# Kernel tuning notes

Measured on AMD Instinct MI355X. Metric: run time of the kernel, lower is better.

Reference implementation:

```python
import jax, jax.numpy as jnp
import numpy as np

B, N, H, L, K, R = 1024, 64, 128, 4, 16, 20
CUTOFF = 5.0
GAMMA = 10.0   # RBF width
N_TYPES = 10

def _rn(k, shape, scale):
    return jax.random.normal(k, shape, jnp.float32) * scale

def setup_inputs():
    key = jax.random.key(0)
    ks = jax.random.split(key, 16)
    z = lambda *s: jnp.zeros(s, jnp.float32)
    return {
        "positions": _rn(ks[0], (B, N, 3), 2.0),
        "atomic_numbers": jax.random.randint(ks[1], (B, N), 0, N_TYPES),
        "atom_embed": _rn(ks[2], (N_TYPES, H // 4), 0.1),
        "pos_W": _rn(ks[3], (3, 3 * H // 4), 0.5),
        "pos_b": z(3 * H // 4),
        "msg_W": _rn(ks[4], (L, 2 * H + R, H), (2 * H + R) ** -0.5),
        "msg_b": z(L, H),
        "upd_W": _rn(ks[5], (L, H, H), H ** -0.5),
        "upd_b": z(L, H),
        "gself_W": _rn(ks[6], (L, H, H), H ** -0.5),
        "gmean_W": _rn(ks[7], (L, H, H), H ** -0.5),
        "g_b": z(L, H),
        "fus_W": _rn(ks[8], (L, 2 * H, H), (2 * H) ** -0.5),
        "fus_b": z(L, H),
        "ln_g": jnp.ones((L, H), jnp.float32),
        "ln_b": z(L, H),
        "cb_W1": _rn(ks[9], (L, H, 4 * H), H ** -0.5),
        "cb_b1": z(L, 4 * H),
        "cb_W2": _rn(ks[10], (L, 4 * H, H), (4 * H) ** -0.5),
        "cb_b2": z(L, H),
        "fo_W1": _rn(ks[11], (H, H), H ** -0.5),
        "fo_b1": z(H),
        "fo_W2": _rn(ks[12], (H, 3), H ** -0.5),
        "fo_b2": z(3),
    }

def _ln(x, g, b):
    m = x.mean(-1, keepdims=True)
    v = ((x - m) ** 2).mean(-1, keepdims=True)
    return (x - m) * jax.lax.rsqrt(v + 1e-5) * g + b

def reference(positions, atomic_numbers, atom_embed, pos_W, pos_b, msg_W, msg_b,
              upd_W, upd_b, gself_W, gmean_W, g_b, fus_W, fus_b, ln_g, ln_b,
              cb_W1, cb_b1, cb_W2, cb_b2, fo_W1, fo_b1, fo_W2, fo_b2):
    silu = jax.nn.silu
    Bb, Nn, _ = positions.shape
    # embeddings: atom type (H/4) || position (3H/4)
    h = jnp.concatenate([atom_embed[atomic_numbers], positions @ pos_W + pos_b], -1)  # [B,N,H]
    # kNN graph from positions (static across layers since positions are fixed)
    diff = positions[:, :, None, :] - positions[:, None, :, :]
    d2 = jnp.sum(diff * diff, -1) + jnp.eye(Nn, dtype=positions.dtype) * 1e9  # exclude self
    neg_d2, idx = jax.lax.top_k(-d2, K)                       # [B,N,K]
    d = jnp.sqrt(jnp.maximum(-neg_d2, 1e-12))
    centers = jnp.linspace(0.0, CUTOFF, R).astype(positions.dtype)
    rbf = jnp.exp(-GAMMA * (d[..., None] - centers) ** 2)     # [B,N,K,R]
    env = (0.5 * (jnp.cos(jnp.pi * d / CUTOFF) + 1.0) * (d < CUTOFF))[..., None]  # cosine cutoff
    idx_flat = idx.reshape(Bb, Nn * K)
    for i in range(msg_W.shape[0]):
        # local MPNN: gather neighbors, message MLP on [h_i, h_j, rbf], envelope, sum
        h_j = jnp.take_along_axis(h, idx_flat[:, :, None], axis=1).reshape(Bb, Nn, K, -1)
        h_i = jnp.broadcast_to(h[:, :, None, :], h_j.shape)
        m = silu(jnp.concatenate([h_i, h_j, rbf], -1) @ msg_W[i] + msg_b[i]) * env
        local = h + silu(m.sum(2) @ upd_W[i] + upd_b[i])
        # Clifford mean-field: self transform + global-mean transform
        glob = silu(h @ gself_W[i] + h.mean(1, keepdims=True) @ gmean_W[i] + g_b[i])
        # fusion (dropout is identity at inference)
        fused = silu(jnp.concatenate([local, glob], -1) @ fus_W[i] + fus_b[i])
        # Clifford block: pre-LN residual MLP
        x = _ln(fused, ln_g[i], ln_b[i])
        h = fused + silu(x @ cb_W1[i] + cb_b1[i]) @ cb_W2[i] + cb_b2[i]
    return silu(h @ fo_W1 + fo_b1) @ fo_W2 + fo_b2  # [B,N,3] forces
```

## Files before the change

### kernel.cpp

```cpp
#include <hip/hip_runtime.h>

typedef unsigned short ushort_t;
typedef unsigned int uint_t;
typedef unsigned long long ull_t;
typedef __attribute__((ext_vector_type(8))) short short8;
typedef __attribute__((ext_vector_type(4))) float f32x4;

#define B_ 1024
#define N_ 64
#define H_ 128
#define NT 512

#define IMG_WI 0
#define IMG_WJ 16384
#define IMG_UW 32768
#define IMG_GS 49152
#define IMG_FT 65536
#define IMG_FB 81920
#define IMG_C1 98304
#define IMG_C2 163840
#define IMG_GMT 229376
#define IMG_RW 245760
#define IMG_L 249856
#define IMG_FO 999424
#define WS_WEIGHTS (2u*1024u*1024u)
#define KNN_STRIDE 12288u

__device__ __forceinline__ ushort_t f2bf(float f) {
    uint_t u = __float_as_uint(f);
    return (ushort_t)((u + 0x7fffu + ((u >> 16) & 1u)) >> 16);
}
__device__ __forceinline__ float bf2f(ushort_t u) {
    union { uint_t i; float f; } v; v.i = ((uint_t)u) << 16; return v.f;
}
__device__ __forceinline__ float siluf(float x) { return x / (1.0f + __expf(-x)); }

__device__ __forceinline__ int sidx(int m, int k) {
    return m * H_ + (((k >> 3) ^ (m & 7)) << 3) + (k & 7);
}
__device__ __forceinline__ int fragoff(int m, int ch) {
    return m * H_ + ((ch ^ (m & 7)) << 3);
}

extern "C" __global__ __launch_bounds__(256)
void convert_weights(const float* __restrict__ msg_W, const float* __restrict__ upd_W,
                     const float* __restrict__ gself_W, const float* __restrict__ fus_W,
                     const float* __restrict__ cb_W1, const float* __restrict__ cb_W2,
                     const float* __restrict__ gmean_W, const float* __restrict__ fo_W1,
                     ushort_t* __restrict__ wimg)
{
    const int g = blockIdx.x;
    if (g >= 244) {
        int st = g - 244;
        ushort_t* dst = wimg + IMG_FO + st * 4096;
        for (int e = 0; e < 16; ++e) {
            int q = threadIdx.x * 16 + e;
            int n = q >> 7, k = q & 127;
            dst[q] = f2bf(fo_W1[(size_t)k * 128 + st * 32 + n]);
        }
        return;
    }
    const int l = g / 61, r = g - l * 61;
    ushort_t* base = wimg + l * IMG_L;
    if (r == 60) {
        const float* W = msg_W + l * 35328 + 256 * 128;
        ushort_t* dst = base + IMG_RW;
        for (int e = 0; e < 16; ++e) {
            int q = threadIdx.x * 16 + e;
            int sub = q >> 10, n = (q >> 5) & 31, k = q & 31;
            dst[q] = f2bf(k < 20 ? W[(size_t)k * 128 + sub * 32 + n] : 0.0f);
        }
        return;
    }
    const float* W; int ld = 128, k0 = 0, c0, off, st;
    if      (r < 4)  { W = msg_W + l * 35328;            st = r;      off = IMG_WI;  c0 = st * 32; }
    else if (r < 8)  { W = msg_W + l * 35328;  k0 = 128; st = r - 4;  off = IMG_WJ;  c0 = st * 32; }
    else if (r < 12) { W = upd_W + l * 16384;            st = r - 8;  off = IMG_UW;  c0 = st * 32; }
    else if (r < 16) { W = gself_W + l * 16384;          st = r - 12; off = IMG_GS;  c0 = st * 32; }
    else if (r < 20) { W = fus_W + l * 32768;            st = r - 16; off = IMG_FT;  c0 = st * 32; }
    else if (r < 24) { W = fus_W + l * 32768;  k0 = 128; st = r - 20; off = IMG_FB;  c0 = st * 32; }
    else if (r < 40) { W = cb_W1 + l * 65536;  ld = 512; st = r - 24; off = IMG_C1;  c0 = st * 32; }
    else if (r < 56) { int j = (r - 40) >> 2; W = cb_W2 + l * 65536; k0 = j * 128;
                       st = r - 40; off = IMG_C2; c0 = ((r - 40) & 3) * 32; }
    else             { W = gmean_W + l * 16384;          st = r - 56; off = IMG_GMT; c0 = st * 32; }
    ushort_t* dst = base + off + st * 4096;
    for (int e = 0; e < 16; ++e) {
        int q = threadIdx.x * 16 + e;
        int n = q >> 7, k = q & 127;
        dst[q] = f2bf(W[(size_t)(k0 + k) * ld + c0 + n]);
    }
}

extern "C" __global__ __launch_bounds__(64)
void knn_kernel(const float* __restrict__ positions, char* __restrict__ ws)
{
    const int b = blockIdx.x, lane = threadIdx.x;
    float px = positions[b * 192 + lane * 3 + 0];
    float py = positions[b * 192 + lane * 3 + 1];
    float pz = positions[b * 192 + lane * 3 + 2];
    float* kd = (float*)(ws + WS_WEIGHTS + (size_t)b * KNN_STRIDE);
    float* ke = kd + 1024;
    ushort_t* ki = (ushort_t*)(ke + 1024);
    for (int n = 0; n < 64; ++n) {
        float dx = __fsub_rn(__shfl(px, n), px);
        float dy = __fsub_rn(__shfl(py, n), py);
        float dz = __fsub_rn(__shfl(pz, n), pz);
        float d2 = __fadd_rn(__fadd_rn(__fmul_rn(dx, dx), __fmul_rn(dy, dy)), __fmul_rn(dz, dz));
        if (lane == n) d2 = 1e30f;
        float sd = 0.f; int si = 0;
        for (int k = 0; k < 16; ++k) {
            float dmin = d2;
            #pragma unroll
            for (int o = 1; o < 64; o <<= 1) dmin = fminf(dmin, __shfl_xor(dmin, o));
            ull_t mask = __ballot(d2 == dmin);
            int widx = __ffsll(mask) - 1;
            if (lane == widx) d2 = 1e30f;
            if (lane == k) { si = widx; sd = dmin; }
        }
        if (lane < 16) {
            float dd = sqrtf(fmaxf(sd, 1e-12f));
            kd[n * 16 + lane] = dd;
            ke[n * 16 + lane] = (dd < 5.0f) ? 0.5f * (__cosf(0.62831853071795864769f * dd) + 1.0f) : 0.0f;
            ki[n * 16 + lane] = (ushort_t)si;
        }
    }
}

#define HFS 132
struct __align__(16) Smem {
    ushort_t T1[N_ * H_];
    ushort_t T2[N_ * H_];
    float Hf[N_ * HFS];
    float d[1024];
    float env[1024];
    ushort_t idx[1024];
    char u[2048];
};

__device__ __forceinline__ f32x4 gemm_s(const short8 a[4], const ushort_t* __restrict__ img,
                                        int s, int nl, int quad)
{
    short8 b0 = *(const short8*)(img + s * 4096 + nl * 128 + (0 * 4 + quad) * 8);
    short8 b1 = *(const short8*)(img + s * 4096 + nl * 128 + (1 * 4 + quad) * 8);
    short8 b2 = *(const short8*)(img + s * 4096 + nl * 128 + (2 * 4 + quad) * 8);
    short8 b3 = *(const short8*)(img + s * 4096 + nl * 128 + (3 * 4 + quad) * 8);
    f32x4 c = {0.f, 0.f, 0.f, 0.f};
    c = __builtin_amdgcn_mfma_f32_16x16x32_bf16(a[0], b0, c, 0, 0, 0);
    c = __builtin_amdgcn_mfma_f32_16x16x32_bf16(a[1], b1, c, 0, 0, 0);
    c = __builtin_amdgcn_mfma_f32_16x16x32_bf16(a[2], b2, c, 0, 0, 0);
    c = __builtin_amdgcn_mfma_f32_16x16x32_bf16(a[3], b3, c, 0, 0, 0);
    return c;
}
__device__ __forceinline__ f32x4 gemm_s_acc(const short8 a[4], const ushort_t* __restrict__ img,
                                            int s, int nl, int quad, f32x4 c)
{
    short8 b0 = *(const short8*)(img + s * 4096 + nl * 128 + (0 * 4 + quad) * 8);
    short8 b1 = *(const short8*)(img + s * 4096 + nl * 128 + (1 * 4 + quad) * 8);
    short8 b2 = *(const short8*)(img + s * 4096 + nl * 128 + (2 * 4 + quad) * 8);
    short8 b3 = *(const short8*)(img + s * 4096 + nl * 128 + (3 * 4 + quad) * 8);
    c = __builtin_amdgcn_mfma_f32_16x16x32_bf16(a[0], b0, c, 0, 0, 0);
    c = __builtin_amdgcn_mfma_f32_16x16x32_bf16(a[1], b1, c, 0, 0, 0);
    c = __builtin_amdgcn_mfma_f32_16x16x32_bf16(a[2], b2, c, 0, 0, 0);
    c = __builtin_amdgcn_mfma_f32_16x16x32_bf16(a[3], b3, c, 0, 0, 0);
    return c;
}
__device__ __forceinline__ void loadA(const ushort_t* __restrict__ X, int mrow, int quad, short8 a[4]) {
    #pragma unroll
    for (int kc = 0; kc < 4; ++kc) a[kc] = *(const short8*)&X[fragoff(mrow, kc * 4 + quad)];
}
__device__ __forceinline__ void buildA(const float* __restrict__ Hf, int mrow, int quad, short8 a[4]) {
    #pragma unroll
    for (int kc = 0; kc < 4; ++kc) {
        const float* p = Hf + mrow * HFS + (kc * 4 + quad) * 8;
        float4 u0 = *(const float4*)p;
        float4 u1 = *(const float4*)(p + 4);
        short8 v;
        v[0] = (short)f2bf(u0.x); v[1] = (short)f2bf(u0.y);
        v[2] = (short)f2bf(u0.z); v[3] = (short)f2bf(u0.w);
        v[4] = (short)f2bf(u1.x); v[5] = (short)f2bf(u1.y);
        v[6] = (short)f2bf(u1.z); v[7] = (short)f2bf(u1.w);
        a[kc] = v;
    }
}

extern "C" __global__ __launch_bounds__(NT, 4)
void md17_fused_kernel(
    const float* __restrict__ positions, const int* __restrict__ atomic_numbers,
    const float* __restrict__ atom_embed, const float* __restrict__ pos_W,
    const float* __restrict__ pos_b,
    const float* __restrict__ msg_b, const float* __restrict__ upd_b,
    const float* __restrict__ g_b, const float* __restrict__ fus_b,
    const float* __restrict__ ln_g, const float* __restrict__ ln_b,
    const float* __restrict__ cb_b1, const float* __restrict__ cb_b2,
    const float* __restrict__ fo_b1,
    const float* __restrict__ fo_W2, const float* __restrict__ fo_b2,
    char* __restrict__ ws, float* __restrict__ out)
{
    __shared__ Smem sm;
    const int b = blockIdx.x;
    const int tid = threadIdx.x;
    const int wave = tid >> 6, lane = tid & 63;
    const int quad = lane >> 4, l15 = lane & 15;
    const int Mt = wave >> 1;
    const int mrow = Mt * 16 + l15;
    const int nl = (wave & 1) * 16 + l15;

    const ushort_t* wimg = (const ushort_t*)ws;
    float* spos = (float*)sm.u;
    ushort_t* part = (ushort_t*)sm.u;
    float* hmean = (float*)(sm.u + 1024);
    float* gvec  = (float*)(sm.u + 1536);
    float2* lnb  = (float2*)sm.u;

    {
        const char* kb = ws + WS_WEIGHTS + (size_t)b * KNN_STRIDE;
        const float* kd = (const float*)kb;
        const float* ke = (const float*)(kb + 4096);
        const uint_t* ki = (const uint_t*)(kb + 8192);
        for (int t = tid; t < 1024; t += NT) { sm.d[t] = kd[t]; sm.env[t] = ke[t]; }
        ((uint_t*)sm.idx)[tid] = ki[tid];
        if (tid < 192) spos[tid] = positions[b * 192 + tid];
    }
    __syncthreads();

    for (int t = tid; t < N_ * H_; t += NT) {
        int n = t >> 7, f = t & 127;
        float v;
        if (f < 32) {
            v = atom_embed[atomic_numbers[b * N_ + n] * 32 + f];
        } else {
            int j = f - 32;
            v = pos_b[j];
            #pragma unroll
            for (int c = 0; c < 3; ++c)
                v = fmaf(spos[n * 3 + c], pos_W[c * 96 + j], v);
        }
        sm.Hf[n * HFS + f] = v;
        sm.T1[sidx(n, f)] = f2bf(v);
    }
    __syncthreads();

    #pragma unroll 1
    for (int l = 0; l < 4; ++l) {
        const ushort_t* wl = wimg + l * IMG_L;
        const float* mb  = msg_b + l * H_;
        const float* ub  = upd_b + l * H_;
        const float* gb  = g_b + l * H_;
        const float* fb  = fus_b + l * H_;
        const float* lg  = ln_g + l * H_;
        const float* lb  = ln_b + l * H_;
        const float* c1b = cb_b1 + l * 4 * H_;
        const float* c2b = cb_b2 + l * H_;

        short8 a_h[4];
        #pragma unroll
        for (int s = 0; s < 4; ++s) {
            int col = s * 32 + nl;
            const float* hp = sm.Hf + (Mt * 16 + quad * 4) * HFS + col;
            float p = hp[0] + hp[HFS] + hp[2 * HFS] + hp[3 * HFS];
            p += __shfl_xor(p, 16);
            p += __shfl_xor(p, 32);
            if (quad == 0) part[Mt * 128 + col] = f2bf(p);
        }
        loadA(sm.T1, mrow, quad, a_h);
        __syncthreads();

        if (tid < H_)
            hmean[tid] = (bf2f(part[tid]) + bf2f(part[128 + tid])
                        + bf2f(part[256 + tid]) + bf2f(part[384 + tid])) * (1.0f / 64.0f);
        __syncthreads();

        if (tid < H_) {
            float s = gb[tid];
            const ushort_t* wrow = wl + IMG_GMT + tid * 128;
            for (int c = 0; c < 128; c += 8) {
                short8 w = *(const short8*)(wrow + c);
                #pragma unroll
                for (int i = 0; i < 8; ++i) s = fmaf(hmean[c + i], bf2f((ushort_t)w[i]), s);
            }
            gvec[tid] = s;
        }
        #pragma unroll
        for (int s = 0; s < 4; ++s) {
            f32x4 c = gemm_s(a_h, wl + IMG_WI, s, nl, quad);
            int col = s * 32 + nl; float bv = mb[col];
            #pragma unroll
            for (int r = 0; r < 4; ++r)
                sm.T1[sidx(Mt * 16 + quad * 4 + r, col)] = f2bf(c[r] + bv);
        }
        #pragma unroll
        for (int s = 0; s < 4; ++s) {
            f32x4 c = gemm_s(a_h, wl + IMG_WJ, s, nl, quad);
            int col = s * 32 + nl;
            #pragma unroll
            for (int r = 0; r < 4; ++r)
                sm.T2[sidx(Mt * 16 + quad * 4 + r, col)] = f2bf(c[r]);
        }
        __syncthreads();

        {
            float ccv[8];
            #pragma unroll
            for (int j = 0; j < 8; ++j)
                ccv[j] = (float)((double)(quad * 8 + j) * (5.0 / 19.0));
            #pragma unroll 1
            for (int g = 0; g < 16; ++g) {
                int n = g * 4 + Mt;
                int jv[4]; float ev[4];
                #pragma unroll
                for (int r = 0; r < 4; ++r) {
                    int k = quad * 4 + r;
                    jv[r] = sm.idx[n * 16 + k];
                    ev[r] = sm.env[n * 16 + k];
                }
                float ddm = sm.d[n * 16 + l15];
                short8 arb;
                #pragma unroll
                for (int j = 0; j < 8; ++j) {
                    float t2 = ddm - ccv[j];
                    float rv = __expf(-10.0f * t2 * t2);
                    arb[j] = (short)((quad * 8 + j) < 20 ? f2bf(rv) : (ushort_t)0);
                }
                #pragma unroll
                for (int s = 0; s < 4; ++s) {
                    short8 brw = *(const short8*)(wl + IMG_RW + s * 1024 + nl * 32 + quad * 8);
                    f32x4 c = {0.f, 0.f, 0.f, 0.f};
                    c = __builtin_amdgcn_mfma_f32_16x16x32_bf16(arb, brw, c, 0, 0, 0);
                    int col = s * 32 + nl;
                    float ai = bf2f(sm.T1[sidx(n, col)]);
                    float acc = 0.f;
                    #pragma unroll
                    for (int r = 0; r < 4; ++r) {
                        float gm = bf2f(sm.T2[sidx(jv[r], col)]);
                        acc = fmaf(siluf(ai + gm + c[r]), ev[r], acc);
                    }
                    acc += __shfl_xor(acc, 16);
                    acc += __shfl_xor(acc, 32);
                    if (quad == 0) sm.T1[sidx(n, col)] = f2bf(acc);
                }
            }
        }
        __syncthreads();

        short8 a_m[4]; loadA(sm.T1, mrow, quad, a_m);
        __syncthreads();

        #pragma unroll
        for (int s = 0; s < 4; ++s) {
            f32x4 c = gemm_s(a_m, wl + IMG_UW, s, nl, quad);
            int col = s * 32 + nl; float bv = ub[col];
            #pragma unroll
            for (int r = 0; r < 4; ++r) {
                int row = Mt * 16 + quad * 4 + r;
                sm.T2[sidx(row, col)] = f2bf(sm.Hf[row * HFS + col] + siluf(c[r] + bv));
            }
        }
        {
            short8 a_hh[4]; buildA(sm.Hf, mrow, quad, a_hh);
            #pragma unroll
            for (int s = 0; s < 4; ++s) {
                f32x4 c = gemm_s(a_hh, wl + IMG_GS, s, nl, quad);
                int col = s * 32 + nl; float gv = gvec[col];
                #pragma unroll
                for (int r = 0; r < 4; ++r)
                    sm.T1[sidx(Mt * 16 + quad * 4 + r, col)] = f2bf(siluf(c[r] + gv));
            }
        }
        __syncthreads();

        {
            short8 a_t[4];
            loadA(sm.T2, mrow, quad, a_t);
            #pragma unroll
            for (int s = 0; s < 4; ++s) {
                f32x4 c = gemm_s(a_t, wl + IMG_FT, s, nl, quad);
                int col = s * 32 + nl;
                int rb = (Mt * 16 + quad * 4) * HFS + col;
                sm.Hf[rb] = c[0]; sm.Hf[rb + HFS] = c[1];
                sm.Hf[rb + 2 * HFS] = c[2]; sm.Hf[rb + 3 * HFS] = c[3];
            }
            loadA(sm.T1, mrow, quad, a_t);
            float sr0 = 0.f, sr1 = 0.f, sr2 = 0.f, sr3 = 0.f;
            float qr0 = 0.f, qr1 = 0.f, qr2 = 0.f, qr3 = 0.f;
            #pragma unroll
            for (int s = 0; s < 4; ++s) {
                f32x4 c = gemm_s(a_t, wl + IMG_FB, s, nl, quad);
                int col = s * 32 + nl; float bv = fb[col];
                int rb = (Mt * 16 + quad * 4) * HFS + col;
                float v0 = siluf(sm.Hf[rb] + c[0] + bv);
                float v1 = siluf(sm.Hf[rb + HFS] + c[1] + bv);
                float v2 = siluf(sm.Hf[rb + 2 * HFS] + c[2] + bv);
                float v3 = siluf(sm.Hf[rb + 3 * HFS] + c[3] + bv);
                sm.Hf[rb] = v0; sm.Hf[rb + HFS] = v1;
                sm.Hf[rb + 2 * HFS] = v2; sm.Hf[rb + 3 * HFS] = v3;
                sr0 += v0; sr1 += v1; sr2 += v2; sr3 += v3;
                qr0 += v0 * v0; qr1 += v1 * v1; qr2 += v2 * v2; qr3 += v3 * v3;
            }
            #pragma unroll
            for (int o = 1; o < 16; o <<= 1) {
                sr0 += __shfl_xor(sr0, o); qr0 += __shfl_xor(qr0, o);
                sr1 += __shfl_xor(sr1, o); qr1 += __shfl_xor(qr1, o);
                sr2 += __shfl_xor(sr2, o); qr2 += __shfl_xor(qr2, o);
                sr3 += __shfl_xor(sr3, o); qr3 += __shfl_xor(qr3, o);
            }
            if (l15 == 0) {
                int base = (Mt * 16 + quad * 4) * 2 + (wave & 1);
                lnb[base]     = make_float2(sr0, qr0);
                lnb[base + 2] = make_float2(sr1, qr1);
                lnb[base + 4] = make_float2(sr2, qr2);
                lnb[base + 6] = make_float2(sr3, qr3);
            }
        }
        __syncthreads();

        #pragma unroll
        for (int r = 0; r < 4; ++r) {
            int row = Mt * 16 + quad * 4 + r;
            float2 h0 = lnb[row * 2], h1 = lnb[row * 2 + 1];
            float mu = (h0.x + h1.x) * (1.0f / 128.0f);
            float var = (h0.y + h1.y) * (1.0f / 128.0f) - mu * mu;
            float rs = rsqrtf(var + 1e-5f);
            #pragma unroll
            for (int s = 0; s < 4; ++s) {
                int col = s * 32 + nl;
                sm.T1[sidx(row, col)] = f2bf((sm.Hf[row * HFS + col] - mu) * rs * lg[col] + lb[col]);
            }
        }
        __syncthreads();

        {
            f32x4 acc2[4];
            #pragma unroll
            for (int s = 0; s < 4; ++s) acc2[s] = (f32x4){0.f, 0.f, 0.f, 0.f};
            #pragma unroll 1
            for (int j = 0; j < 4; ++j) {
                {
                    short8 a_x[4]; loadA(sm.T1, mrow, quad, a_x);
                    #pragma unroll
                    for (int s = 0; s < 4; ++s) {
                        f32x4 c = gemm_s(a_x, wl + IMG_C1 + j * 16384, s, nl, quad);
                        int col = s * 32 + nl; float bv = c1b[j * H_ + col];
                        #pragma unroll
                        for (int r = 0; r < 4; ++r)
                            sm.T2[sidx(Mt * 16 + quad * 4 + r, col)] = f2bf(siluf(c[r] + bv));
                    }
                }
                __syncthreads();
                {
                    short8 a_t[4]; loadA(sm.T2, mrow, quad, a_t);
                    #pragma unroll
                    for (int s = 0; s < 4; ++s)
                        acc2[s] = gemm_s_acc(a_t, wl + IMG_C2 + j * 16384, s, nl, quad, acc2[s]);
                }
                __syncthreads();
            }

            #pragma unroll
            for (int s = 0; s < 4; ++s) {
                int col = s * 32 + nl; float bv = c2b[col];
                #pragma unroll
                for (int r = 0; r < 4; ++r) {
                    int row = Mt * 16 + quad * 4 + r;
                    float v = sm.Hf[row * HFS + col] + acc2[s][r] + bv;
                    sm.Hf[row * HFS + col] = v;
                    sm.T1[sidx(row, col)] = f2bf(v);
                }
            }
        }
        __syncthreads();
    }

    {
        short8 a_f[4]; loadA(sm.T1, mrow, quad, a_f);
        #pragma unroll
        for (int s = 0; s < 4; ++s) {
            f32x4 c = gemm_s(a_f, wimg + IMG_FO, s, nl, quad);
            int col = s * 32 + nl; float bv = fo_b1[col];
            #pragma unroll
            for (int r = 0; r < 4; ++r)
                sm.T2[sidx(Mt * 16 + quad * 4 + r, col)] = f2bf(siluf(c[r] + bv));
        }
    }
    __syncthreads();
    if (tid < N_ * 3) {
        int n = tid / 3, j = tid - n * 3;
        float s = fo_b2[j];
        for (int c = 0; c < H_; ++c)
            s = fmaf(bf2f(sm.T2[sidx(n, c)]), fo_W2[c * 3 + j], s);
        out[b * N_ * 3 + tid] = s;
    }
}

extern "C" void kernel_launch(void* const* d_in, const int* in_sizes, int n_in,
                              void* d_out, int out_size, void* d_ws, size_t ws_size,
                              hipStream_t stream) {
    (void)in_sizes; (void)n_in; (void)out_size; (void)ws_size;
    convert_weights<<<248, 256, 0, stream>>>(
        (const float*)d_in[5], (const float*)d_in[7], (const float*)d_in[9],
        (const float*)d_in[12], (const float*)d_in[16], (const float*)d_in[18],
        (const float*)d_in[10], (const float*)d_in[20], (ushort_t*)d_ws);
    knn_kernel<<<B_, 64, 0, stream>>>((const float*)d_in[0], (char*)d_ws);
    md17_fused_kernel<<<B_, NT, 0, stream>>>(
        (const float*)d_in[0], (const int*)d_in[1],
        (const float*)d_in[2], (const float*)d_in[3], (const float*)d_in[4],
        (const float*)d_in[6], (const float*)d_in[8],
        (const float*)d_in[11], (const float*)d_in[13],
        (const float*)d_in[14], (const float*)d_in[15],
        (const float*)d_in[17], (const float*)d_in[19],
        (const float*)d_in[21],
        (const float*)d_in[22], (const float*)d_in[23],
        (char*)d_ws, (float*)d_out);
}
```

Baseline: 1.490 ms.

## Give each wave full 16-row strips to drop most block barriers

The block shrinks from 8 to 4 waves per batch element. Each wave now owns 16 complete rows across all 128 output columns, so row-local steps no longer need __syncthreads. These steps are the update and self-transform GEMMs, the fusion and LayerNorm row statistics, and the 4-chunk residual MLP; LayerNorm stats are reduced with shuffles instead of going through shared memory. The cost is half as many waves per block, more accumulator registers per thread (8 output tiles), and a lower occupancy hint in launch bounds.

After: 1.479 ms. About the same (-0.7%).

```diff
diff --git a/kernel.cpp b/kernel.cpp
--- a/kernel.cpp
+++ b/kernel.cpp
@@ -9,7 +9,7 @@
 #define B_ 1024
 #define N_ 64
 #define H_ 128
-#define NT 512
+#define NT 256
 
 #define IMG_WI 0
 #define IMG_WJ 16384
@@ -138,12 +138,13 @@
 };
 
 __device__ __forceinline__ f32x4 gemm_s(const short8 a[4], const ushort_t* __restrict__ img,
-                                        int s, int nl, int quad)
+                                        int s, int l15, int quad)
 {
-    short8 b0 = *(const short8*)(img + s * 4096 + nl * 128 + (0 * 4 + quad) * 8);
-    short8 b1 = *(const short8*)(img + s * 4096 + nl * 128 + (1 * 4 + quad) * 8);
-    short8 b2 = *(const short8*)(img + s * 4096 + nl * 128 + (2 * 4 + quad) * 8);
-    short8 b3 = *(const short8*)(img + s * 4096 + nl * 128 + (3 * 4 + quad) * 8);
+    const ushort_t* base = img + ((s >> 1) << 12) + ((((s & 1) << 4) + l15) << 7) + quad * 8;
+    short8 b0 = *(const short8*)(base);
+    short8 b1 = *(const short8*)(base + 32);
+    short8 b2 = *(const short8*)(base + 64);
+    short8 b3 = *(const short8*)(base + 96);
     f32x4 c = {0.f, 0.f, 0.f, 0.f};
     c = __builtin_amdgcn_mfma_f32_16x16x32_bf16(a[0], b0, c, 0, 0, 0);
     c = __builtin_amdgcn_mfma_f32_16x16x32_bf16(a[1], b1, c, 0, 0, 0);
@@ -152,12 +153,13 @@
     return c;
 }
 __device__ __forceinline__ f32x4 gemm_s_acc(const short8 a[4], const ushort_t* __restrict__ img,
-                                            int s, int nl, int quad, f32x4 c)
+                                            int s, int l15, int quad, f32x4 c)
 {
-    short8 b0 = *(const short8*)(img + s * 4096 + nl * 128 + (0 * 4 + quad) * 8);
-    short8 b1 = *(const short8*)(img + s * 4096 + nl * 128 + (1 * 4 + quad) * 8);
-    short8 b2 = *(const short8*)(img + s * 4096 + nl * 128 + (2 * 4 + quad) * 8);
-    short8 b3 = *(const short8*)(img + s * 4096 + nl * 128 + (3 * 4 + quad) * 8);
+    const ushort_t* base = img + ((s >> 1) << 12) + ((((s & 1) << 4) + l15) << 7) + quad * 8;
+    short8 b0 = *(const short8*)(base);
+    short8 b1 = *(const short8*)(base + 32);
+    short8 b2 = *(const short8*)(base + 64);
+    short8 b3 = *(const short8*)(base + 96);
     c = __builtin_amdgcn_mfma_f32_16x16x32_bf16(a[0], b0, c, 0, 0, 0);
     c = __builtin_amdgcn_mfma_f32_16x16x32_bf16(a[1], b1, c, 0, 0, 0);
     c = __builtin_amdgcn_mfma_f32_16x16x32_bf16(a[2], b2, c, 0, 0, 0);
@@ -183,7 +185,7 @@
     }
 }
 
-extern "C" __global__ __launch_bounds__(NT, 4)
+extern "C" __global__ __launch_bounds__(NT, 2)
 void md17_fused_kernel(
     const float* __restrict__ positions, const int* __restrict__ atomic_numbers,
     const float* __restrict__ atom_embed, const float* __restrict__ pos_W,
@@ -201,16 +203,14 @@
     const int tid = threadIdx.x;
     const int wave = tid >> 6, lane = tid & 63;
     const int quad = lane >> 4, l15 = lane & 15;
-    const int Mt = wave >> 1;
-    const int mrow = Mt * 16 + l15;
-    const int nl = (wave & 1) * 16 + l15;
+    const int mrow = wave * 16 + l15;
+    const int rbase = wave * 16 + quad * 4;
 
     const ushort_t* wimg = (const ushort_t*)ws;
     float* spos = (float*)sm.u;
     ushort_t* part = (ushort_t*)sm.u;
     float* hmean = (float*)(sm.u + 1024);
     float* gvec  = (float*)(sm.u + 1536);
-    float2* lnb  = (float2*)sm.u;
 
     {
         const char* kb = ws + WS_WEIGHTS + (size_t)b * KNN_STRIDE;
@@ -218,11 +218,10 @@
         const float* ke = (const float*)(kb + 4096);
         const uint_t* ki = (const uint_t*)(kb + 8192);
         for (int t = tid; t < 1024; t += NT) { sm.d[t] = kd[t]; sm.env[t] = ke[t]; }
-        ((uint_t*)sm.idx)[tid] = ki[tid];
+        for (int t = tid; t < 512; t += NT) ((uint_t*)sm.idx)[t] = ki[t];
         if (tid < 192) spos[tid] = positions[b * 192 + tid];
     }
     __syncthreads();
-
     for (int t = tid; t < N_ * H_; t += NT) {
         int n = t >> 7, f = t & 127;
         float v;
@@ -252,19 +251,16 @@
         const float* c1b = cb_b1 + l * 4 * H_;
         const float* c2b = cb_b2 + l * H_;
 
-        short8 a_h[4];
         #pragma unroll
-        for (int s = 0; s < 4; ++s) {
-            int col = s * 32 + nl;
-            const float* hp = sm.Hf + (Mt * 16 + quad * 4) * HFS + col;
+        for (int s = 0; s < 8; ++s) {
+            int col = s * 16 + l15;
+            const float* hp = sm.Hf + rbase * HFS + col;
             float p = hp[0] + hp[HFS] + hp[2 * HFS] + hp[3 * HFS];
             p += __shfl_xor(p, 16);
             p += __shfl_xor(p, 32);
-            if (quad == 0) part[Mt * 128 + col] = f2bf(p);
-        }
-        loadA(sm.T1, mrow, quad, a_h);
+            if (quad == 0) part[wave * 128 + col] = f2bf(p);
+        }
         __syncthreads();
-
         if (tid < H_)
             hmean[tid] = (bf2f(part[tid]) + bf2f(part[128 + tid])
                         + bf2f(part[256 + tid]) + bf2f(part[384 + tid])) * (1.0f / 64.0f);
@@ -280,21 +276,24 @@
             }
             gvec[tid] = s;
         }
-        #pragma unroll
-        for (int s = 0; s < 4; ++s) {
-            f32x4 c = gemm_s(a_h, wl + IMG_WI, s, nl, quad);
-            int col = s * 32 + nl; float bv = mb[col];
-            #pragma unroll
-            for (int r = 0; r < 4; ++r)
-                sm.T1[sidx(Mt * 16 + quad * 4 + r, col)] = f2bf(c[r] + bv);
-        }
-        #pragma unroll
-        for (int s = 0; s < 4; ++s) {
-            f32x4 c = gemm_s(a_h, wl + IMG_WJ, s, nl, quad);
-            int col = s * 32 + nl;
-            #pragma unroll
-            for (int r = 0; r < 4; ++r)
-                sm.T2[sidx(Mt * 16 + quad * 4 + r, col)] = f2bf(c[r]);
+        {
+            short8 a_h[4]; loadA(sm.T1, mrow, quad, a_h);
+            #pragma unroll
+            for (int s = 0; s < 8; ++s) {
+                f32x4 c = gemm_s(a_h, wl + IMG_WI, s, l15, quad);
+                int col = s * 16 + l15; float bv = mb[col];
+                #pragma unroll
+                for (int r = 0; r < 4; ++r)
+                    sm.T1[sidx(rbase + r, col)] = f2bf(c[r] + bv);
+            }
+            #pragma unroll
+            for (int s = 0; s < 8; ++s) {
+                f32x4 c = gemm_s(a_h, wl + IMG_WJ, s, l15, quad);
+                int col = s * 16 + l15;
+                #pragma unroll
+                for (int r = 0; r < 4; ++r)
+                    sm.T2[sidx(rbase + r, col)] = f2bf(c[r]);
+            }
         }
         __syncthreads();
 
@@ -305,7 +304,7 @@
                 ccv[j] = (float)((double)(quad * 8 + j) * (5.0 / 19.0));
             #pragma unroll 1
             for (int g = 0; g < 16; ++g) {
-                int n = g * 4 + Mt;
+                int n = wave * 16 + g;
                 int jv[4]; float ev[4];
                 #pragma unroll
                 for (int r = 0; r < 4; ++r) {
@@ -322,11 +321,13 @@
                     arb[j] = (short)((quad * 8 + j) < 20 ? f2bf(rv) : (ushort_t)0);
                 }
                 #pragma unroll
-                for (int s = 0; s < 4; ++s) {
-                    short8 brw = *(const short8*)(wl + IMG_RW + s * 1024 + nl * 32 + quad * 8);
+                for (int s = 0; s < 8; ++s) {
+                    int col = s * 16 + l15;
+                    const ushort_t* rbase_p = wl + IMG_RW + ((s >> 1) << 10)
+                                            + ((((s & 1) << 4) + l15) << 5) + quad * 8;
+                    short8 brw = *(const short8*)rbase_p;
                     f32x4 c = {0.f, 0.f, 0.f, 0.f};
                     c = __builtin_amdgcn_mfma_f32_16x16x32_bf16(arb, brw, c, 0, 0, 0);
-                    int col = s * 32 + nl;
                     float ai = bf2f(sm.T1[sidx(n, col)]);
                     float acc = 0.f;
                     #pragma unroll
@@ -342,152 +343,128 @@
         }
         __syncthreads();
 
-        short8 a_m[4]; loadA(sm.T1, mrow, quad, a_m);
-        __syncthreads();
-
-        #pragma unroll
-        for (int s = 0; s < 4; ++s) {
-            f32x4 c = gemm_s(a_m, wl + IMG_UW, s, nl, quad);
-            int col = s * 32 + nl; float bv = ub[col];
-            #pragma unroll
-            for (int r = 0; r < 4; ++r) {
-                int row = Mt * 16 + quad * 4 + r;
-                sm.T2[sidx(row, col)] = f2bf(sm.Hf[row * HFS + col] + siluf(c[r] + bv));
-            }
-        }
+
         {
+            short8 a_m[4]; loadA(sm.T1, mrow, quad, a_m);
+            #pragma unroll
+            for (int s = 0; s < 8; ++s) {
+                f32x4 c = gemm_s(a_m, wl + IMG_UW, s, l15, quad);
+                int col = s * 16 + l15; float bv = ub[col];
+                #pragma unroll
+                for (int r = 0; r < 4; ++r)
+                    sm.T2[sidx(rbase + r, col)] = f2bf(sm.Hf[(rbase + r) * HFS + col] + siluf(c[r] + bv));
+            }
             short8 a_hh[4]; buildA(sm.Hf, mrow, quad, a_hh);
             #pragma unroll
-            for (int s = 0; s < 4; ++s) {
-                f32x4 c = gemm_s(a_hh, wl + IMG_GS, s, nl, quad);
-                int col = s * 32 + nl; float gv = gvec[col];
+            for (int s = 0; s < 8; ++s) {
+                f32x4 c = gemm_s(a_hh, wl + IMG_GS, s, l15, quad);
+                int col = s * 16 + l15; float gv = gvec[col];
                 #pragma unroll
                 for (int r = 0; r < 4; ++r)
-                    sm.T1[sidx(Mt * 16 + quad * 4 + r, col)] = f2bf(siluf(c[r] + gv));
-            }
-        }
-        __syncthreads();
-
+                    sm.T1[sidx(rbase + r, col)] = f2bf(siluf(c[r] + gv));
+            }
+        }
+
+        float sr[4] = {0.f, 0.f, 0.f, 0.f}, qr[4] = {0.f, 0.f, 0.f, 0.f};
         {
             short8 a_t[4];
             loadA(sm.T2, mrow, quad, a_t);
             #pragma unroll
-            for (int s = 0; s < 4; ++s) {
-                f32x4 c = gemm_s(a_t, wl + IMG_FT, s, nl, quad);
-                int col = s * 32 + nl;
-                int rb = (Mt * 16 + quad * 4) * HFS + col;
+            for (int s = 0; s < 8; ++s) {
+                f32x4 c = gemm_s(a_t, wl + IMG_FT, s, l15, quad);
+                int col = s * 16 + l15;
+                int rb = rbase * HFS + col;
                 sm.Hf[rb] = c[0]; sm.Hf[rb + HFS] = c[1];
                 sm.Hf[rb + 2 * HFS] = c[2]; sm.Hf[rb + 3 * HFS] = c[3];
             }
             loadA(sm.T1, mrow, quad, a_t);
-            float sr0 = 0.f, sr1 = 0.f, sr2 = 0.f, sr3 = 0.f;
-            float qr0 = 0.f, qr1 = 0.f, qr2 = 0.f, qr3 = 0.f;
-            #pragma unroll
-            for (int s = 0; s < 4; ++s) {
-                f32x4 c = gemm_s(a_t, wl + IMG_FB, s, nl, quad);
-                int col = s * 32 + nl; float bv = fb[col];
-                int rb = (Mt * 16 + quad * 4) * HFS + col;
-                float v0 = siluf(sm.Hf[rb] + c[0] + bv);
-                float v1 = siluf(sm.Hf[rb + HFS] + c[1] + bv);
-                float v2 = siluf(sm.Hf[rb + 2 * HFS] + c[2] + bv);
-                float v3 = siluf(sm.Hf[rb + 3 * HFS] + c[3] + bv);
-                sm.Hf[rb] = v0; sm.Hf[rb + HFS] = v1;
-                sm.Hf[rb + 2 * HFS] = v2; sm.Hf[rb + 3 * HFS] = v3;
-                sr0 += v0; sr1 += v1; sr2 += v2; sr3 += v3;
-                qr0 += v0 * v0; qr1 += v1 * v1; qr2 += v2 * v2; qr3 += v3 * v3;
+            #pragma unroll
+            for (int s = 0; s < 8; ++s) {
+                f32x4 c = gemm_s(a_t, wl + IMG_FB, s, l15, quad);
+                int col = s * 16 + l15; float bv = fb[col];
+                int rb = rbase * HFS + col;
+                #pragma unroll
+                for (int r = 0; r < 4; ++r) {
+                    float v = siluf(sm.Hf[rb + r * HFS] + c[r] + bv);
+                    sm.Hf[rb + r * HFS] = v;
+                    sr[r] += v; qr[r] += v * v;
+                }
             }
             #pragma unroll
             for (int o = 1; o < 16; o <<= 1) {
-                sr0 += __shfl_xor(sr0, o); qr0 += __shfl_xor(qr0, o);
-                sr1 += __shfl_xor(sr1, o); qr1 += __shfl_xor(qr1, o);
-                sr2 += __shfl_xor(sr2, o); qr2 += __shfl_xor(qr2, o);
-                sr3 += __shfl_xor(sr3, o); qr3 += __shfl_xor(qr3, o);
-            }
-            if (l15 == 0) {
-                int base = (Mt * 16 + quad * 4) * 2 + (wave & 1);
-                lnb[base]     = make_float2(sr0, qr0);
-                lnb[base + 2] = make_float2(sr1, qr1);
-                lnb[base + 4] = make_float2(sr2, qr2);
-                lnb[base + 6] = make_float2(sr3, qr3);
-            }
-        }
-        __syncthreads();
+                #pragma unroll
+                for (int r = 0; r < 4; ++r) {
+                    sr[r] += __shfl_xor(sr[r], o);
+                    qr[r] += __shfl_xor(qr[r], o);
+                }
+            }
+        }
 
         #pragma unroll
         for (int r = 0; r < 4; ++r) {
-            int row = Mt * 16 + quad * 4 + r;
-            float2 h0 = lnb[row * 2], h1 = lnb[row * 2 + 1];
-            float mu = (h0.x + h1.x) * (1.0f / 128.0f);
-            float var = (h0.y + h1.y) * (1.0f / 128.0f) - mu * mu;
+            float mu = sr[r] * (1.0f / 128.0f);
+            float var = qr[r] * (1.0f / 128.0f) - mu * mu;
             float rs = rsqrtf(var + 1e-5f);
-            #pragma unroll
-            for (int s = 0; s < 4; ++s) {
-                int col = s * 32 + nl;
+            int row = rbase + r;
+            #pragma unroll
+            for (int s = 0; s < 8; ++s) {
+                int col = s * 16 + l15;
                 sm.T1[sidx(row, col)] = f2bf((sm.Hf[row * HFS + col] - mu) * rs * lg[col] + lb[col]);
             }
         }
-        __syncthreads();
 
         {
-            f32x4 acc2[4];
-            #pragma unroll
-            for (int s = 0; s < 4; ++s) acc2[s] = (f32x4){0.f, 0.f, 0.f, 0.f};
+            short8 a_x[4]; loadA(sm.T1, mrow, quad, a_x);
+            f32x4 acc2[8];
+            #pragma unroll
+            for (int s = 0; s < 8; ++s) acc2[s] = (f32x4){0.f, 0.f, 0.f, 0.f};
             #pragma unroll 1
             for (int j = 0; j < 4; ++j) {
-                {
-                    short8 a_x[4]; loadA(sm.T1, mrow, quad, a_x);
+                #pragma unroll
+                for (int s = 0; s < 8; ++s) {
+                    f32x4 c = gemm_s(a_x, wl + IMG_C1 + j * 16384, s, l15, quad);
+                    int col = s * 16 + l15; float bv = c1b[j * H_ + col];
                     #pragma unroll
-                    for (int s = 0; s < 4; ++s) {
-                        f32x4 c = gemm_s(a_x, wl + IMG_C1 + j * 16384, s, nl, quad);
-                        int col = s * 32 + nl; float bv = c1b[j * H_ + col];
-                        #pragma unroll
-                        for (int r = 0; r < 4; ++r)
-                            sm.T2[sidx(Mt * 16 + quad * 4 + r, col)] = f2bf(siluf(c[r] + bv));
-                    }
-                }
-                __syncthreads();
-                {
-                    short8 a_t[4]; loadA(sm.T2, mrow, quad, a_t);
-                    #pragma unroll
-                    for (int s = 0; s < 4; ++s)
-                        acc2[s] = gemm_s_acc(a_t, wl + IMG_C2 + j * 16384, s, nl, quad, acc2[s]);
-                }
-                __syncthreads();
-            }
-
-            #pragma unroll
-            for (int s = 0; s < 4; ++s) {
-                int col = s * 32 + nl; float bv = c2b[col];
+                    for (int r = 0; r < 4; ++r)
+                        sm.T2[sidx(rbase + r, col)] = f2bf(siluf(c[r] + bv));
+                }
+                short8 a_t[4]; loadA(sm.T2, mrow, quad, a_t);
+                #pragma unroll
+                for (int s = 0; s < 8; ++s)
+                    acc2[s] = gemm_s_acc(a_t, wl + IMG_C2 + j * 16384, s, l15, quad, acc2[s]);
+            }
+            #pragma unroll
+            for (int s = 0; s < 8; ++s) {
+                int col = s * 16 + l15; float bv = c2b[col];
                 #pragma unroll
                 for (int r = 0; r < 4; ++r) {
-                    int row = Mt * 16 + quad * 4 + r;
+                    int row = rbase + r;
                     float v = sm.Hf[row * HFS + col] + acc2[s][r] + bv;
                     sm.Hf[row * HFS + col] = v;
                     sm.T1[sidx(row, col)] = f2bf(v);
                 }
             }
         }
-        __syncthreads();
     }
 
     {
         short8 a_f[4]; loadA(sm.T1, mrow, quad, a_f);
         #pragma unroll
-        for (int s = 0; s < 4; ++s) {
-            f32x4 c = gemm_s(a_f, wimg + IMG_FO, s, nl, quad);
-            int col = s * 32 + nl; float bv = fo_b1[col];
+        for (int s = 0; s < 8; ++s) {
+            f32x4 c = gemm_s(a_f, wimg + IMG_FO, s, l15, quad);
+            int col = s * 16 + l15; float bv = fo_b1[col];
             #pragma unroll
             for (int r = 0; r < 4; ++r)
-                sm.T2[sidx(Mt * 16 + quad * 4 + r, col)] = f2bf(siluf(c[r] + bv));
+                sm.T2[sidx(rbase + r, col)] = f2bf(siluf(c[r] + bv));
         }
     }
     __syncthreads();
-    if (tid < N_ * 3) {
+    if (tid < 192) {
         int n = tid / 3, j = tid - n * 3;
         float s = fo_b2[j];
         for (int c = 0; c < H_; ++c)
             s = fmaf(bf2f(sm.T2[sidx(n, c)]), fo_W2[c * 3 + j], s);
-        out[b * N_ * 3 + tid] = s;
+        out[b * 192 + tid] = s;
     }
 }
 
```
